# Kernel tuning notes

Measured on AMD Instinct MI355X. Metric: run time of the kernel, lower is better.

Reference implementation:

```python
import jax, jax.numpy as jnp
import numpy as np

D_MODEL = 1024
NUM_HEADS = 16
DEPTH = D_MODEL // NUM_HEADS


def setup_inputs() -> dict:
    key = jax.random.key(0)
    ks = jax.random.split(key, 9)
    B, S = 2, 2048
    s = 1.0 / np.sqrt(D_MODEL)
    return {
        "x": jax.random.normal(ks[0], (B, S, D_MODEL), dtype=jnp.float32),
        "wq": jax.random.normal(ks[1], (D_MODEL, D_MODEL), dtype=jnp.float32) * s,
        "bq": jnp.zeros((D_MODEL,), dtype=jnp.float32),
        "wk": jax.random.normal(ks[2], (D_MODEL, D_MODEL), dtype=jnp.float32) * s,
        "bk": jnp.zeros((D_MODEL,), dtype=jnp.float32),
        "wv": jax.random.normal(ks[3], (D_MODEL, D_MODEL), dtype=jnp.float32) * s,
        "bv": jnp.zeros((D_MODEL,), dtype=jnp.float32),
        "wo": jax.random.normal(ks[4], (D_MODEL, D_MODEL), dtype=jnp.float32) * s,
        "bo": jnp.zeros((D_MODEL,), dtype=jnp.float32),
    }


def _split_heads(t):
    # [B, S, D] -> [B, H, S, depth]
    B, S, _ = t.shape
    return t.reshape(B, S, NUM_HEADS, DEPTH).transpose(0, 2, 1, 3)


def reference(x, wq, bq, wk, bk, wv, bv, wo, bo):
    B, S, _ = x.shape
    q = _split_heads(x @ wq + bq)
    k = _split_heads(x @ wk + bk)
    v = _split_heads(x @ wv + bv)
    scale = 1.0 / jnp.sqrt(jnp.asarray(DEPTH, dtype=x.dtype))
    logits = jnp.einsum("bhsd,bhtd->bhst", q, k) * scale  # [B,H,S,S]
    attn = jax.nn.softmax(logits, axis=-1)
    ctx = jnp.einsum("bhst,bhtd->bhsd", attn, v)  # [B,H,S,depth]
    concat = ctx.transpose(0, 2, 1, 3).reshape(B, S, D_MODEL)
    return concat @ wo + bo
```

## Files before the change

### kernel.cpp

```cpp
#include <hip/hip_runtime.h>
#include <hip/hip_bf16.h>

typedef __bf16 bf16;
typedef __bf16 bf16x4 __attribute__((ext_vector_type(4)));
typedef __bf16 bf16x8 __attribute__((ext_vector_type(8)));
typedef float f32x4 __attribute__((ext_vector_type(4)));

typedef __attribute__((address_space(3))) void lds_void;
typedef const __attribute__((address_space(1))) void gbl_void;

#define D_MODEL 1024
#define NHEAD 16
#define DEPTH 64
#define SEQ 2048
#define BATCH 2
#define NTOK (BATCH * SEQ)

#define Q_SCALE 0.18033688f

__global__ __launch_bounds__(256) void prep(const float* __restrict__ w0,
                                            const float* __restrict__ w1,
                                            const float* __restrict__ w2,
                                            const float* __restrict__ w3,
                                            const float* __restrict__ x,
                                            bf16* __restrict__ wtb,
                                            bf16* __restrict__ xb) {
    int z = blockIdx.z;
    int tx = threadIdx.x, ty = threadIdx.y;
    if (z < 4) {
        const float* w = (z == 0) ? w0 : (z == 1) ? w1 : (z == 2) ? w2 : w3;
        bf16* d = wtb + (size_t)z * D_MODEL * D_MODEL;
        __shared__ float tile[32][33];
        int c0 = blockIdx.x * 32;
        int r0 = blockIdx.y * 32;
#pragma unroll
        for (int i = 0; i < 4; i++)
            tile[ty + i * 8][tx] = w[(size_t)(r0 + ty + i * 8) * D_MODEL + c0 + tx];
        __syncthreads();
#pragma unroll
        for (int i = 0; i < 4; i++)
            d[(size_t)(c0 + ty + i * 8) * D_MODEL + r0 + tx] = (bf16)tile[tx][ty + i * 8];
    } else {
        int t = ty * 32 + tx;
        size_t i = ((size_t)(z - 4) * 1024 + blockIdx.y * 32 + blockIdx.x) * 256 + t;
        float4 v = ((const float4*)x)[i];
        bf16x4 o = {(bf16)v.x, (bf16)v.y, (bf16)v.z, (bf16)v.w};
        *(bf16x4*)&xb[i * 4] = o;
    }
}

__global__ __launch_bounds__(512, 2) void qkv_gemm(const bf16* __restrict__ xb,
                                                   const bf16* __restrict__ wtb,
                                                   const float* __restrict__ bq,
                                                   const float* __restrict__ bk,
                                                   const float* __restrict__ bv,
                                                   bf16* __restrict__ q,
                                                   bf16* __restrict__ k,
                                                   bf16* __restrict__ v) {
    __shared__ bf16 sm[65536];

    const int flat = blockIdx.x;
    const int wg = (flat & 7) * 24 + (flat >> 3);
    const int mt = wg & 15, nt = wg >> 4;
    const int row0 = mt << 8;
    const int z = nt >> 2;
    const int nb = (nt & 3) << 8;

    const int tid = threadIdx.x;
    const int lane = tid & 63, wave = tid >> 6;
    const int wm = wave >> 2, wn = wave & 3;
    const int quad = lane >> 4, l16 = lane & 15;
    const int kch = ((quad ^ ((l16 >> 1) & 3)) << 3);

    const int srow = lane >> 2;
    const int scg = (lane & 3) ^ ((lane >> 3) & 3);
    const int stDst = wave * 1024 + lane * 8;

    const bf16* Ag = xb + (size_t)(row0 + wave * 32 + srow) * D_MODEL + scg * 8;
    const bf16* Bg = wtb + (size_t)z * D_MODEL * D_MODEL
                   + (size_t)(nb + wave * 32 + srow) * D_MODEL + scg * 8;

    f32x4 acc[8][4] = {};
    bf16x8 bfr[4];

#define GLL(SRC, DST) __builtin_amdgcn_global_load_lds((gbl_void*)(SRC), (lds_void*)(DST), 16, 0, 0)
#define STG_A(T_, KQ_, BUF_) { \
    const bf16* s_ = Ag + (T_) * 64 + (KQ_) * 32; \
    bf16* d_ = sm + (BUF_) * 16384 + (KQ_) * 8192 + stDst; \
    GLL(s_, d_); GLL(s_ + 16 * D_MODEL, d_ + 512); }
#define STG_B(T_, KQ_, BUF_) { \
    const bf16* s_ = Bg + (T_) * 64 + (KQ_) * 32; \
    bf16* d_ = sm + 32768 + (BUF_) * 16384 + (KQ_) * 8192 + stDst; \
    GLL(s_, d_); GLL(s_ + 16 * D_MODEL, d_ + 512); }
#define WAIT6 { asm volatile("s_waitcnt vmcnt(6)" ::: "memory"); }
#define NOW

#define PHASE(BUF_, KQ_, MQ_, STG_STMT, WAIT_STMT) { \
    bf16x8 af[4]; \
    const int ab_ = (BUF_) * 16384 + (KQ_) * 8192 + (wm * 128 + (MQ_) * 64 + l16) * 32 + kch; \
    _Pragma("unroll") \
    for (int i_ = 0; i_ < 4; i_++) af[i_] = *(const bf16x8*)&sm[ab_ + i_ * 512]; \
    if ((MQ_) == 0) { \
        const int bb_ = 32768 + (BUF_) * 16384 + (KQ_) * 8192 + (wn * 64 + l16) * 32 + kch; \
        _Pragma("unroll") \
        for (int j_ = 0; j_ < 4; j_++) bfr[j_] = *(const bf16x8*)&sm[bb_ + j_ * 512]; \
    } \
    STG_STMT; \
    WAIT_STMT; \
    __builtin_amdgcn_sched_barrier(0); \
    __builtin_amdgcn_s_barrier(); \
    __builtin_amdgcn_s_setprio(1); \
    _Pragma("unroll") \
    for (int i_ = 0; i_ < 4; i_++) \
        _Pragma("unroll") \
        for (int j_ = 0; j_ < 4; j_++) \
            acc[(MQ_) * 4 + i_][j_] = __builtin_amdgcn_mfma_f32_16x16x32_bf16( \
                af[i_], bfr[j_], acc[(MQ_) * 4 + i_][j_], 0, 0, 0); \
    __builtin_amdgcn_s_setprio(0); \
    __builtin_amdgcn_sched_barrier(0); \
    __builtin_amdgcn_s_barrier(); }

    STG_B(0, 0, 0);
    STG_A(0, 0, 0);
    STG_B(0, 1, 0);
    STG_A(0, 1, 0);
    asm volatile("s_waitcnt vmcnt(4)" ::: "memory");
    STG_B(1, 0, 1);
    STG_A(1, 0, 1);
    STG_B(1, 1, 1);
    asm volatile("s_waitcnt vmcnt(6)" ::: "memory");
    __builtin_amdgcn_sched_barrier(0);
    __builtin_amdgcn_s_barrier();

#pragma unroll 1
    for (int it = 0; it < 8; ++it) {
        const int t1 = 2 * it + 1;
        const int t2 = (2 * it + 2) & 15;
        const int t3 = (2 * it + 3) & 15;
        PHASE(0, 0, 0, STG_A(t1, 1, 1), NOW)
        PHASE(0, 0, 1, STG_B(t2, 0, 0), NOW)
        PHASE(0, 1, 0, STG_A(t2, 0, 0), NOW)
        PHASE(0, 1, 1, STG_B(t2, 1, 0), WAIT6)
        PHASE(1, 0, 0, STG_A(t2, 1, 0), NOW)
        PHASE(1, 0, 1, STG_B(t3, 0, 1), NOW)
        PHASE(1, 1, 0, STG_A(t3, 0, 1), NOW)
        PHASE(1, 1, 1, STG_B(t3, 1, 1), WAIT6)
    }

#undef PHASE
#undef WAIT6
#undef NOW
#undef STG_A
#undef STG_B
#undef GLL

    const float* bias = (z == 0) ? bq : (z == 1) ? bk : bv;
    const int bI = row0 >> 11;
    const int sBase = row0 & 2047;
    if (z < 2) {
        bf16* dst = (z == 0) ? q : k;
        const float scl = (z == 0) ? Q_SCALE : 1.0f;
#pragma unroll
        for (int j = 0; j < 4; j++) {
            const int f = nb + wn * 64 + j * 16 + l16;
            const float bi = bias[f];
            const int hh = f >> 6, d = f & 63;
            bf16* dcol = dst + ((size_t)(bI * NHEAD + hh) * SEQ) * DEPTH + d;
#pragma unroll
            for (int mi = 0; mi < 8; mi++) {
                const int s0 = sBase + wm * 128 + (mi >> 2) * 64 + (mi & 3) * 16 + quad * 4;
#pragma unroll
                for (int r = 0; r < 4; r++)
                    dcol[(size_t)(s0 + r) * DEPTH] = (bf16)((acc[mi][j][r] + bi) * scl);
            }
        }
    } else {
#pragma unroll
        for (int j = 0; j < 4; j++) {
            const int f = nb + wn * 64 + j * 16 + l16;
            const float bi = bias[f];
            const int hh = f >> 6, d = f & 63;
            bf16* vrow = v + ((size_t)(bI * NHEAD + hh) * DEPTH + d) * SEQ;
#pragma unroll
            for (int mi = 0; mi < 8; mi++) {
                const int s0 = sBase + wm * 128 + (mi >> 2) * 64 + (mi & 3) * 16 + quad * 4;
                f32x4 a = acc[mi][j];
                bf16x4 ob = {(bf16)(a[0] + bi), (bf16)(a[1] + bi),
                             (bf16)(a[2] + bi), (bf16)(a[3] + bi)};
                *(bf16x4*)&vrow[s0] = ob;
            }
        }
    }
}

__global__ __launch_bounds__(256) void attn(const bf16* __restrict__ q,
                                            const bf16* __restrict__ k,
                                            const bf16* __restrict__ v,
                                            bf16* __restrict__ ctx) {
    __shared__ __align__(16) char smem[36864];
    const int tid = threadIdx.x;
    const int lane = tid & 63, wave = tid >> 6;
    const int quad = lane >> 4, l16 = lane & 15;
    const int bh = blockIdx.x;
    const int q0 = blockIdx.y * 64;
    const size_t hb = (size_t)bh * SEQ * DEPTH;
    const bf16* qh = q + hb;
    const bf16* kh = k + hb;
    const bf16* vh = v + hb;

    bf16x8 bq_[4][2];
#pragma unroll
    for (int n = 0; n < 4; n++) {
        int qrow = q0 + n * 16 + l16;
#pragma unroll
        for (int c = 0; c < 2; c++)
            bq_[n][c] = *(const bf16x8*)&qh[(size_t)qrow * DEPTH + c * 32 + quad * 8];
    }

    const int klane = (wave * 32 + ((l16 >> 2) << 3) + (l16 & 3)) * DEPTH + quad * 8;
    const int vlane = l16 * SEQ + wave * 32 + quad * 8;

    f32x4 ov[4][4] = {};
    f32x4 lv = {};

    bf16x8 ka[2][2], kb2[2][2];
    bf16x8 va[4], vb[4];

#define LOADK(KF, T_) { \
    const bf16* kp_ = kh + (size_t)(T_) * DEPTH + klane; \
    KF[0][0] = *(const bf16x8*)(kp_); \
    KF[0][1] = *(const bf16x8*)(kp_ + 32); \
    KF[1][0] = *(const bf16x8*)(kp_ + 256); \
    KF[1][1] = *(const bf16x8*)(kp_ + 288); }

#define LOADV(VF, T_) { \
    const bf16* vp_ = vh + vlane + (T_); \
    VF[0] = *(const bf16x8*)(vp_); \
    VF[1] = *(const bf16x8*)(vp_ + 16 * SEQ); \
    VF[2] = *(const bf16x8*)(vp_ + 32 * SEQ); \
    VF[3] = *(const bf16x8*)(vp_ + 48 * SEQ); }

#define COMPUTE(KF, VF) { \
    f32x4 s0[4] = {}, s1[4] = {}; \
    _Pragma("unroll") \
    for (int n_ = 0; n_ < 4; n_++) { \
        s0[n_] = __builtin_amdgcn_mfma_f32_16x16x32_bf16(KF[0][0], bq_[n_][0], s0[n_], 0, 0, 0); \
        s0[n_] = __builtin_amdgcn_mfma_f32_16x16x32_bf16(KF[0][1], bq_[n_][1], s0[n_], 0, 0, 0); \
        s1[n_] = __builtin_amdgcn_mfma_f32_16x16x32_bf16(KF[1][0], bq_[n_][0], s1[n_], 0, 0, 0); \
        s1[n_] = __builtin_amdgcn_mfma_f32_16x16x32_bf16(KF[1][1], bq_[n_][1], s1[n_], 0, 0, 0); \
    } \
    bf16x8 pb[4]; \
    _Pragma("unroll") \
    for (int n_ = 0; n_ < 4; n_++) { \
        float e0 = __builtin_amdgcn_exp2f(s0[n_][0]); \
        float e1 = __builtin_amdgcn_exp2f(s0[n_][1]); \
        float e2 = __builtin_amdgcn_exp2f(s0[n_][2]); \
        float e3 = __builtin_amdgcn_exp2f(s0[n_][3]); \
        float e4 = __builtin_amdgcn_exp2f(s1[n_][0]); \
        float e5 = __builtin_amdgcn_exp2f(s1[n_][1]); \
        float e6 = __builtin_amdgcn_exp2f(s1[n_][2]); \
        float e7 = __builtin_amdgcn_exp2f(s1[n_][3]); \
        pb[n_][0] = (bf16)e0; pb[n_][1] = (bf16)e1; \
        pb[n_][2] = (bf16)e2; pb[n_][3] = (bf16)e3; \
        pb[n_][4] = (bf16)e4; pb[n_][5] = (bf16)e5; \
        pb[n_][6] = (bf16)e6; pb[n_][7] = (bf16)e7; \
        lv[n_] += ((e0 + e1) + (e2 + e3)) + ((e4 + e5) + (e6 + e7)); \
    } \
    _Pragma("unroll") \
    for (int t_ = 0; t_ < 4; t_++) \
        _Pragma("unroll") \
        for (int n_ = 0; n_ < 4; n_++) \
            ov[t_][n_] = __builtin_amdgcn_mfma_f32_16x16x32_bf16(VF[t_], pb[n_], ov[t_][n_], 0, 0, 0); }

    LOADK(ka, 0);
#pragma unroll 1
    for (int tt = 0; tt < SEQ; tt += 256) {
        LOADV(va, tt);
        LOADK(kb2, tt + 128);
        __builtin_amdgcn_sched_barrier(0);
        COMPUTE(ka, va);
        LOADV(vb, tt + 128);
        LOADK(ka, (tt + 256) & (SEQ - 1));
        __builtin_amdgcn_sched_barrier(0);
        COMPUTE(kb2, vb);
    }
#undef COMPUTE
#undef LOADV
#undef LOADK

    f32x4* Red  = (f32x4*)smem;
    f32x4* Lred = (f32x4*)(smem + 32768);
    __syncthreads();
#pragma unroll
    for (int tt = 0; tt < 8; tt++)
        Red[(tt * 4 + wave) * 64 + lane] = ov[tt >> 2][tt & 3];
    Lred[wave * 64 + lane] = lv;
    __syncthreads();
    f32x4 ls = {};
#pragma unroll
    for (int w_ = 0; w_ < 4; w_++)
#pragma unroll
        for (int qd = 0; qd < 4; qd++)
            ls += Lred[w_ * 64 + qd * 16 + l16];
    const int b = bh >> 4, hh = bh & 15;
    const int wb1 = wave & 1;
#pragma unroll
    for (int u = 0; u < 2; u++) {
        int tt = wave * 2 + u;
        f32x4 sv = Red[(tt * 4 + 0) * 64 + lane] + Red[(tt * 4 + 1) * 64 + lane]
                 + Red[(tt * 4 + 2) * 64 + lane] + Red[(tt * 4 + 3) * 64 + lane];
        int n = wb1 * 2 + u, t = wave >> 1;
        float iv = 1.0f / (wb1 ? ls[2 + u] : ls[u]);
        bf16x4 ob = {(bf16)(sv[0] * iv), (bf16)(sv[1] * iv),
                     (bf16)(sv[2] * iv), (bf16)(sv[3] * iv)};
        size_t off = ((size_t)(b * SEQ + q0 + n * 16 + l16)) * D_MODEL
                   + hh * 64 + t * 16 + quad * 4;
        *(bf16x4*)&ctx[off] = ob;
    }
    __syncthreads();
#pragma unroll
    for (int tt = 8; tt < 16; tt++)
        Red[((tt - 8) * 4 + wave) * 64 + lane] = ov[tt >> 2][tt & 3];
    __syncthreads();
#pragma unroll
    for (int u = 0; u < 2; u++) {
        int tt = 8 + wave * 2 + u;
        int rt = tt - 8;
        f32x4 sv = Red[(rt * 4 + 0) * 64 + lane] + Red[(rt * 4 + 1) * 64 + lane]
                 + Red[(rt * 4 + 2) * 64 + lane] + Red[(rt * 4 + 3) * 64 + lane];
        int n = wb1 * 2 + u, t = 2 + (wave >> 1);
        float iv = 1.0f / (wb1 ? ls[2 + u] : ls[u]);
        bf16x4 ob = {(bf16)(sv[0] * iv), (bf16)(sv[1] * iv),
                     (bf16)(sv[2] * iv), (bf16)(sv[3] * iv)};
        size_t off = ((size_t)(b * SEQ + q0 + n * 16 + l16)) * D_MODEL
                   + hh * 64 + t * 16 + quad * 4;
        *(bf16x4*)&ctx[off] = ob;
    }
}

__global__ __launch_bounds__(256) void out_gemm(const bf16* __restrict__ ctx,
                                                const bf16* __restrict__ wot,
                                                const float* __restrict__ bo,
                                                float* __restrict__ out) {
    __shared__ bf16 As[64 * 32];
    __shared__ bf16 Bs[128 * 32];
    const int tid = threadIdx.x;
    const int lane = tid & 63, wave = tid >> 6;
    const int quad = lane >> 4, l16 = lane & 15;
    const int srow = lane >> 2, selem = (lane & 3) * 8;
    int row0 = blockIdx.y * 64, col0 = blockIdx.x * 128;
    f32x4 acc[4][2] = {};

    for (int k0 = 0; k0 < D_MODEL; k0 += 32) {
        __syncthreads();
        {
            const bf16* ga = ctx + (size_t)(row0 + wave * 16 + srow) * D_MODEL + k0 + selem;
            __builtin_amdgcn_global_load_lds((gbl_void*)ga, (lds_void*)(As + wave * 512 + lane * 8), 16, 0, 0);
        }
#pragma unroll
        for (int t = 0; t < 2; t++) {
            int m = wave * 2 + t;
            const bf16* gb = wot + (size_t)(col0 + m * 16 + srow) * D_MODEL + k0 + selem;
            __builtin_amdgcn_global_load_lds((gbl_void*)gb, (lds_void*)(Bs + m * 512 + lane * 8), 16, 0, 0);
        }
        __syncthreads();
        bf16x8 af[4], bfr[2];
#pragma unroll
        for (int i = 0; i < 4; i++)
            af[i] = *(const bf16x8*)&As[(i * 16 + l16) * 32 + quad * 8];
#pragma unroll
        for (int j = 0; j < 2; j++)
            bfr[j] = *(const bf16x8*)&Bs[(wave * 32 + j * 16 + l16) * 32 + quad * 8];
#pragma unroll
        for (int i = 0; i < 4; i++)
#pragma unroll
            for (int j = 0; j < 2; j++)
                acc[i][j] = __builtin_amdgcn_mfma_f32_16x16x32_bf16(af[i], bfr[j], acc[i][j], 0, 0, 0);
    }
#pragma unroll
    for (int i = 0; i < 4; i++)
#pragma unroll
        for (int j = 0; j < 2; j++) {
            int colg = col0 + wave * 32 + j * 16 + l16;
            float bi = bo[colg];
            int rbase = row0 + i * 16 + quad * 4;
#pragma unroll
            for (int r = 0; r < 4; r++)
                out[(size_t)(rbase + r) * D_MODEL + colg] = acc[i][j][r] + bi;
        }
}

extern "C" void kernel_launch(void* const* d_in, const int* in_sizes, int n_in,
                              void* d_out, int out_size, void* d_ws, size_t ws_size,
                              hipStream_t stream) {
    const float* x  = (const float*)d_in[0];
    const float* wq = (const float*)d_in[1];
    const float* bq = (const float*)d_in[2];
    const float* wk = (const float*)d_in[3];
    const float* bk = (const float*)d_in[4];
    const float* wv = (const float*)d_in[5];
    const float* bv = (const float*)d_in[6];
    const float* wo = (const float*)d_in[7];
    const float* bo = (const float*)d_in[8];
    float* out = (float*)d_out;

    const size_t MB = 1024 * 1024;
    char* ws = (char*)d_ws;
    bf16* xb  = (bf16*)(ws);
    bf16* wtb = (bf16*)(ws + 8 * MB);
    bf16* qb  = (bf16*)(ws + 16 * MB);
    bf16* kb  = (bf16*)(ws + 24 * MB);
    bf16* vb  = (bf16*)(ws + 32 * MB);
    bf16* ctx = (bf16*)(ws + 40 * MB);

    prep<<<dim3(32, 32, 8), dim3(32, 8), 0, stream>>>(wq, wk, wv, wo, x, wtb, xb);
    qkv_gemm<<<dim3(192), dim3(512), 0, stream>>>(xb, wtb, bq, bk, bv, qb, kb, vb);
    attn<<<dim3(BATCH * NHEAD, SEQ / 64), 256, 0, stream>>>(qb, kb, vb, ctx);
    out_gemm<<<dim3(8, 64), 256, 0, stream>>>(ctx, wtb + 3 * (size_t)D_MODEL * D_MODEL, bo, out);
}
```

Baseline: 213.2 us.

## Stage attention K/V tiles through LDS with async global_load_lds double buffering

The attention inner loop no longer loads K and V fragments straight from global memory into registers. Each wave now copies its K and V tiles into its own double-buffered LDS region with asynchronous global_load_lds, using XOR swizzles to avoid bank conflicts. Fragments are then read back from LDS, and explicit vmcnt waits overlap the next tile's copy with the current compute. s_setprio is also raised around the MFMA sections. The trade-off is a larger LDS footprint (64KB per block, up from 36KB), which can reduce occupancy, plus extra LDS read traffic.

```diff
diff --git a/kernel.cpp b/kernel.cpp
--- a/kernel.cpp
+++ b/kernel.cpp
@@ -197,7 +197,7 @@
                                             const bf16* __restrict__ k,
                                             const bf16* __restrict__ v,
                                             bf16* __restrict__ ctx) {
-    __shared__ __align__(16) char smem[36864];
+    __shared__ __align__(16) bf16 smb[32768];
     const int tid = threadIdx.x;
     const int lane = tid & 63, wave = tid >> 6;
     const int quad = lane >> 4, l16 = lane & 15;
@@ -217,79 +217,100 @@
             bq_[n][c] = *(const bf16x8*)&qh[(size_t)qrow * DEPTH + c * 32 + quad * 8];
     }
 
-    const int klane = (wave * 32 + ((l16 >> 2) << 3) + (l16 & 3)) * DEPTH + quad * 8;
-    const int vlane = l16 * SEQ + wave * 32 + quad * 8;
-
     f32x4 ov[4][4] = {};
     f32x4 lv = {};
 
-    bf16x8 ka[2][2], kb2[2][2];
-    bf16x8 va[4], vb[4];
-
-#define LOADK(KF, T_) { \
-    const bf16* kp_ = kh + (size_t)(T_) * DEPTH + klane; \
-    KF[0][0] = *(const bf16x8*)(kp_); \
-    KF[0][1] = *(const bf16x8*)(kp_ + 32); \
-    KF[1][0] = *(const bf16x8*)(kp_ + 256); \
-    KF[1][1] = *(const bf16x8*)(kp_ + 288); }
-
-#define LOADV(VF, T_) { \
-    const bf16* vp_ = vh + vlane + (T_); \
-    VF[0] = *(const bf16x8*)(vp_); \
-    VF[1] = *(const bf16x8*)(vp_ + 16 * SEQ); \
-    VF[2] = *(const bf16x8*)(vp_ + 32 * SEQ); \
-    VF[3] = *(const bf16x8*)(vp_ + 48 * SEQ); }
-
-#define COMPUTE(KF, VF) { \
-    f32x4 s0[4] = {}, s1[4] = {}; \
+    const int wb = wave * 8192;
+    const int kchS = (lane & 7) ^ (((lane >> 3) & 3) << 1);
+    const int vchS = (lane & 3) ^ ((lane >> 2) & 3);
+    const int krdL = ((l16 >> 2) << 3) + (l16 & 3);
+    const int ksw = ((l16 & 3) << 1) | ((l16 >> 2) & 1);
+    const int vsw = (quad ^ (l16 & 3)) << 3;
+
+#define GLL(SRC, DST) __builtin_amdgcn_global_load_lds((gbl_void*)(SRC), (lds_void*)(DST), 16, 0, 0)
+
+#define STAGE(BUF_, T_) { \
+    _Pragma("unroll") \
+    for (int o_ = 0; o_ < 4; o_++) { \
+        const bf16* s_ = kh + (size_t)((T_) + wave * 32 + o_ * 8 + (lane >> 3)) * DEPTH \
+                       + ((kchS ^ (o_ & 1)) << 3); \
+        GLL(s_, smb + wb + (BUF_) * 2048 + o_ * 512 + lane * 8); \
+    } \
+    _Pragma("unroll") \
+    for (int o_ = 0; o_ < 4; o_++) { \
+        const bf16* s_ = vh + (size_t)(o_ * 16 + (lane >> 2)) * SEQ + (T_) + wave * 32 \
+                       + (vchS << 3); \
+        GLL(s_, smb + wb + 4096 + (BUF_) * 2048 + o_ * 512 + lane * 8); \
+    } }
+
+#define COMPUTE(BUF_) { \
+    f32x4 s[2][4] = {}; \
+    __builtin_amdgcn_s_setprio(1); \
+    _Pragma("unroll") \
+    for (int c_ = 0; c_ < 2; c_++) \
+        _Pragma("unroll") \
+        for (int h_ = 0; h_ < 2; h_++) { \
+            bf16x8 kf = *(const bf16x8*)&smb[wb + (BUF_) * 2048 + (krdL + h_ * 4) * 64 \
+                                             + ((((c_ << 2) | quad) ^ ksw) << 3)]; \
+            _Pragma("unroll") \
+            for (int n_ = 0; n_ < 4; n_++) \
+                s[h_][n_] = __builtin_amdgcn_mfma_f32_16x16x32_bf16(kf, bq_[n_][c_], s[h_][n_], 0, 0, 0); \
+        } \
+    __builtin_amdgcn_s_setprio(0); \
+    bf16x8 pb[4]; \
     _Pragma("unroll") \
     for (int n_ = 0; n_ < 4; n_++) { \
-        s0[n_] = __builtin_amdgcn_mfma_f32_16x16x32_bf16(KF[0][0], bq_[n_][0], s0[n_], 0, 0, 0); \
-        s0[n_] = __builtin_amdgcn_mfma_f32_16x16x32_bf16(KF[0][1], bq_[n_][1], s0[n_], 0, 0, 0); \
-        s1[n_] = __builtin_amdgcn_mfma_f32_16x16x32_bf16(KF[1][0], bq_[n_][0], s1[n_], 0, 0, 0); \
-        s1[n_] = __builtin_amdgcn_mfma_f32_16x16x32_bf16(KF[1][1], bq_[n_][1], s1[n_], 0, 0, 0); \
-    } \
-    bf16x8 pb[4]; \
-    _Pragma("unroll") \
-    for (int n_ = 0; n_ < 4; n_++) { \
-        float e0 = __builtin_amdgcn_exp2f(s0[n_][0]); \
-        float e1 = __builtin_amdgcn_exp2f(s0[n_][1]); \
-        float e2 = __builtin_amdgcn_exp2f(s0[n_][2]); \
-        float e3 = __builtin_amdgcn_exp2f(s0[n_][3]); \
-        float e4 = __builtin_amdgcn_exp2f(s1[n_][0]); \
-        float e5 = __builtin_amdgcn_exp2f(s1[n_][1]); \
-        float e6 = __builtin_amdgcn_exp2f(s1[n_][2]); \
-        float e7 = __builtin_amdgcn_exp2f(s1[n_][3]); \
+        float e0 = __builtin_amdgcn_exp2f(s[0][n_][0]); \
+        float e1 = __builtin_amdgcn_exp2f(s[0][n_][1]); \
+        float e2 = __builtin_amdgcn_exp2f(s[0][n_][2]); \
+        float e3 = __builtin_amdgcn_exp2f(s[0][n_][3]); \
+        float e4 = __builtin_amdgcn_exp2f(s[1][n_][0]); \
+        float e5 = __builtin_amdgcn_exp2f(s[1][n_][1]); \
+        float e6 = __builtin_amdgcn_exp2f(s[1][n_][2]); \
+        float e7 = __builtin_amdgcn_exp2f(s[1][n_][3]); \
         pb[n_][0] = (bf16)e0; pb[n_][1] = (bf16)e1; \
         pb[n_][2] = (bf16)e2; pb[n_][3] = (bf16)e3; \
         pb[n_][4] = (bf16)e4; pb[n_][5] = (bf16)e5; \
         pb[n_][6] = (bf16)e6; pb[n_][7] = (bf16)e7; \
         lv[n_] += ((e0 + e1) + (e2 + e3)) + ((e4 + e5) + (e6 + e7)); \
     } \
-    _Pragma("unroll") \
-    for (int t_ = 0; t_ < 4; t_++) \
+    __builtin_amdgcn_s_setprio(1); \
+    _Pragma("unroll") \
+    for (int t_ = 0; t_ < 4; t_++) { \
+        bf16x8 vf = *(const bf16x8*)&smb[wb + 4096 + (BUF_) * 2048 + (t_ * 16 + l16) * 32 + vsw]; \
         _Pragma("unroll") \
         for (int n_ = 0; n_ < 4; n_++) \
-            ov[t_][n_] = __builtin_amdgcn_mfma_f32_16x16x32_bf16(VF[t_], pb[n_], ov[t_][n_], 0, 0, 0); }
-
-    LOADK(ka, 0);
+            ov[t_][n_] = __builtin_amdgcn_mfma_f32_16x16x32_bf16(vf, pb[n_], ov[t_][n_], 0, 0, 0); \
+    } \
+    __builtin_amdgcn_s_setprio(0); }
+
+#define WAITV(N_) { asm volatile("s_waitcnt vmcnt(" #N_ ")" ::: "memory"); }
+#define SB0 __builtin_amdgcn_sched_barrier(0)
+
+    STAGE(0, 0);
 #pragma unroll 1
-    for (int tt = 0; tt < SEQ; tt += 256) {
-        LOADV(va, tt);
-        LOADK(kb2, tt + 128);
-        __builtin_amdgcn_sched_barrier(0);
-        COMPUTE(ka, va);
-        LOADV(vb, tt + 128);
-        LOADK(ka, (tt + 256) & (SEQ - 1));
-        __builtin_amdgcn_sched_barrier(0);
-        COMPUTE(kb2, vb);
-    }
+    for (int tt = 0; tt < SEQ - 256; tt += 256) {
+        STAGE(1, tt + 128);
+        WAITV(8); SB0;
+        COMPUTE(0); SB0;
+        STAGE(0, tt + 256);
+        WAITV(8); SB0;
+        COMPUTE(1); SB0;
+    }
+    STAGE(1, SEQ - 128);
+    WAITV(8); SB0;
+    COMPUTE(0); SB0;
+    WAITV(0); SB0;
+    COMPUTE(1);
+
+#undef SB0
+#undef WAITV
 #undef COMPUTE
-#undef LOADV
-#undef LOADK
-
-    f32x4* Red  = (f32x4*)smem;
-    f32x4* Lred = (f32x4*)(smem + 32768);
+#undef STAGE
+#undef GLL
+
+    f32x4* Red  = (f32x4*)smb;
+    f32x4* Lred = (f32x4*)((char*)smb + 32768);
     __syncthreads();
 #pragma unroll
     for (int tt = 0; tt < 8; tt++)
@@ -324,8 +345,7 @@
     __syncthreads();
 #pragma unroll
     for (int u = 0; u < 2; u++) {
-        int tt = 8 + wave * 2 + u;
-        int rt = tt - 8;
+        int rt = wave * 2 + u;
         f32x4 sv = Red[(rt * 4 + 0) * 64 + lane] + Red[(rt * 4 + 1) * 64 + lane]
                  + Red[(rt * 4 + 2) * 64 + lane] + Red[(rt * 4 + 3) * 64 + lane];
         int n = wb1 * 2 + u, t = 2 + (wave >> 1);
```

Result: faster. 187.2 us (-12.2%).
